# Optimization experiments

Measured on AMD Instinct MI355X. Metric: run time of the kernel, lower is better.

Reference implementation:

```python
import jax, jax.numpy as jnp
import numpy as np

QMAX = 255.0  # uint8 range used by KVQuantizer


def setup_inputs() -> dict:
    key = jax.random.key(0)
    k1, k2 = jax.random.split(key)
    B, KVH, D, S = 1, 8, 128, 8192
    keys = jax.random.normal(k1, (B, KVH, 1, D, S), dtype=jnp.float32)
    values = jax.random.normal(k2, (B, KVH, 1, S, D), dtype=jnp.float32)
    return {"keys": keys, "values": values, "mask": 1, "ids_len": S, "kv_seq_len": S}


def _quantize_block(x, axis):
    # torch.aminmax(x, dim=axis, keepdim=True)
    block_min = jnp.min(x, axis=axis, keepdims=True)
    block_max = jnp.max(x, axis=axis, keepdims=True)
    scale = (block_max - block_min) * (1.0 / QMAX)
    x_packed = jnp.round((x - block_min) / scale)  # F16 path: stays float
    # USE_FLOAT16_SCALE_BIAS=True -> half precision scale/bias
    return x_packed, scale.astype(jnp.float16), block_min.astype(jnp.float16)


def reference(keys, values, mask, ids_len, kv_seq_len):
    # causal mask: (1 - tril(ones)) * -128, sliced [:ids_len, :kv_seq_len], * mask, .float()
    row = jnp.arange(ids_len)[:, None]
    col = jnp.arange(kv_seq_len)[None, :]
    attn = (jnp.where(col > row, jnp.int32(-128), jnp.int32(0)) * jnp.int32(mask)).astype(jnp.float32)
    attn = attn[None, None, None]  # [1,1,1,ids_len,kv_seq_len]

    # per-layer KV-cache quantization (keys blocked over head_dim axis -2, values over -1)
    k_packed, k_scale, k_bias = _quantize_block(keys, -2)
    v_packed, v_scale, v_bias = _quantize_block(values, -1)
    return (attn, k_packed, k_scale, k_bias, v_packed, jnp.swapaxes(v_scale, -1, -2), v_bias)
```

## Files before the change

### kernel.cpp

```cpp
#include <hip/hip_runtime.h>
#include <hip/hip_fp16.h>

#define HH 8
#define DD 128
#define SS 8192

typedef float f32x4 __attribute__((ext_vector_type(4)));

#define GROUPS 1024
#define BLOCKS (GROUPS * 25)

__global__ __launch_bounds__(256) void fused_kernel(
    const float* __restrict__ keys, const float* __restrict__ vals,
    const int* __restrict__ maskp,
    float* __restrict__ attn, float* __restrict__ kp, float* __restrict__ ks,
    float* __restrict__ kb, float* __restrict__ vp, float* __restrict__ vs,
    float* __restrict__ vb)
{
    const int tid = threadIdx.x;
    const int b   = blockIdx.x;
    const int g   = b / 25;
    const int rem = b - g * 25;

    if (rem == 0) {
        const int h  = g >> 7;
        const int s0 = (g & 127) << 6;
        const int sq = tid & 15;
        const int dg = tid >> 4;

        const float* base = keys + (size_t)h * DD * SS + (size_t)dg * 8 * SS + s0 + sq * 4;
        f32x4 v[8];
        f32x4 mn4, mx4;
        mn4.x = mn4.y = mn4.z = mn4.w = 3.0e38f;
        mx4.x = mx4.y = mx4.z = mx4.w = -3.0e38f;
#pragma unroll
        for (int j = 0; j < 8; ++j) {
            v[j] = __builtin_nontemporal_load((const f32x4*)(base + (size_t)j * SS));
            mn4.x = fminf(mn4.x, v[j].x); mx4.x = fmaxf(mx4.x, v[j].x);
            mn4.y = fminf(mn4.y, v[j].y); mx4.y = fmaxf(mx4.y, v[j].y);
            mn4.z = fminf(mn4.z, v[j].z); mx4.z = fmaxf(mx4.z, v[j].z);
            mn4.w = fminf(mn4.w, v[j].w); mx4.w = fmaxf(mx4.w, v[j].w);
        }

        __shared__ f32x4 smn[16][16], smx[16][16];
        __shared__ float sinv[64], sbi[64];
        smn[dg][sq] = mn4;
        smx[dg][sq] = mx4;
        __syncthreads();
        if (tid < 64) {
            const int q = tid >> 2, cmp = tid & 3;
            float m = 3.0e38f, M = -3.0e38f;
#pragma unroll
            for (int gg = 0; gg < 16; ++gg) {
                m = fminf(m, ((const float*)&smn[gg][q])[cmp]);
                M = fmaxf(M, ((const float*)&smx[gg][q])[cmp]);
            }
            const float scale = (M - m) * (1.0f / 255.0f);
            sinv[tid] = 1.0f / scale;
            sbi[tid]  = m;
            const int o = h * SS + s0 + tid;
            ks[o] = __half2float(__float2half(scale));
            kb[o] = __half2float(__float2half(m));
        }
        __syncthreads();
        const f32x4 rs = *(const f32x4*)&sinv[sq * 4];
        const f32x4 bi = *(const f32x4*)&sbi[sq * 4];
        float* ob = kp + (size_t)h * DD * SS + (size_t)dg * 8 * SS + s0 + sq * 4;
#pragma unroll
        for (int j = 0; j < 8; ++j) {
            f32x4 o;
            o.x = rintf((v[j].x - bi.x) * rs.x);
            o.y = rintf((v[j].y - bi.y) * rs.y);
            o.z = rintf((v[j].z - bi.z) * rs.z);
            o.w = rintf((v[j].w - bi.w) * rs.w);
            *(f32x4*)(ob + (size_t)j * SS) = o;
        }
    } else if (rem <= 8) {
        const int vbi = g * 8 + (rem - 1);
        const int d4 = tid & 31;
        const int rr = tid >> 5;
        const int R  = vbi * 8 + rr;

        const f32x4 v = __builtin_nontemporal_load((const f32x4*)vals + (size_t)R * 32 + d4);
        float mn = fminf(fminf(v.x, v.y), fminf(v.z, v.w));
        float mx = fmaxf(fmaxf(v.x, v.y), fmaxf(v.z, v.w));
#pragma unroll
        for (int off = 16; off >= 1; off >>= 1) {
            mn = fminf(mn, __shfl_xor(mn, off));
            mx = fmaxf(mx, __shfl_xor(mx, off));
        }
        const float scale = (mx - mn) * (1.0f / 255.0f);
        const float inv   = 1.0f / scale;
        if (d4 == 0) {
            vs[R] = __half2float(__float2half(scale));
            vb[R] = __half2float(__float2half(mn));
        }
        f32x4 o;
        o.x = rintf((v.x - mn) * inv);
        o.y = rintf((v.y - mn) * inv);
        o.z = rintf((v.z - mn) * inv);
        o.w = rintf((v.w - mn) * inv);
        *((f32x4*)vp + (size_t)R * 32 + d4) = o;
    } else {
        const int a = g * 16 + (rem - 9);
        const float hi = (float)(-128 * (*maskp));
        const int base = a * 1024 + tid;
#pragma unroll
        for (int ch = 0; ch < 4; ++ch) {
            const int idx = base + ch * 256;
            const int r = idx >> 11;
            const int c = (idx & 2047) << 2;
            f32x4 v;
            v.x = (c + 0 > r) ? hi : 0.0f;
            v.y = (c + 1 > r) ? hi : 0.0f;
            v.z = (c + 2 > r) ? hi : 0.0f;
            v.w = (c + 3 > r) ? hi : 0.0f;
            *((f32x4*)attn + idx) = v;
        }
    }
}

extern "C" void kernel_launch(void* const* d_in, const int* in_sizes, int n_in,
                              void* d_out, int out_size, void* d_ws, size_t ws_size,
                              hipStream_t stream) {
    const float* keys  = (const float*)d_in[0];
    const float* vals  = (const float*)d_in[1];
    const int*   maskp = (const int*)d_in[2];

    float* out  = (float*)d_out;
    float* attn = out;
    float* kp   = attn + 67108864;
    float* ks   = kp   + 8388608;
    float* kb   = ks   + 65536;
    float* vp   = kb   + 65536;
    float* vs   = vp   + 8388608;
    float* vb   = vs   + 65536;

    fused_kernel<<<dim3(BLOCKS), dim3(256), 0, stream>>>(keys, vals, maskp,
                                                         attn, kp, ks, kb, vp, vs, vb);
}
```

Measured before the change: 386.0 us.

## Split fused interleaved kernel into separate keys, values and attention-mask kernels

Replaces the single fused kernel, which interleaved key, value and mask blocks by block index, with three separate launches. The mask kernel becomes a grid-stride loop with 32 iterations per thread over 2048 blocks, and the value kernel now handles 32 rows per block. This is meant to cut block count and per-block dispatch overhead and to make each kernel's work uniform. In exchange it adds two kernel launches and gives up the overlap of the read-heavy quantization work with the write-only mask fill.

Result: no change. 384.1 us (-0.5%).

```diff
diff --git a/kernel.cpp b/kernel.cpp
--- a/kernel.cpp
+++ b/kernel.cpp
@@ -7,80 +7,92 @@
 
 typedef float f32x4 __attribute__((ext_vector_type(4)));
 
-#define GROUPS 1024
-#define BLOCKS (GROUPS * 25)
+#define ATTN_BLOCKS 2048
+__global__ __launch_bounds__(256) void attn_kernel(const int* __restrict__ maskp,
+                                                   float* __restrict__ out) {
+    const float hi = (float)(-128 * (*maskp));
+    int idx = blockIdx.x * 256 + threadIdx.x;
+#pragma unroll
+    for (int it = 0; it < 32; ++it, idx += ATTN_BLOCKS * 256) {
+        const int r = idx >> 11;
+        const int c = (idx & 2047) << 2;
+        f32x4 v;
+        v.x = (c + 0 > r) ? hi : 0.0f;
+        v.y = (c + 1 > r) ? hi : 0.0f;
+        v.z = (c + 2 > r) ? hi : 0.0f;
+        v.w = (c + 3 > r) ? hi : 0.0f;
+        *((f32x4*)out + idx) = v;
+    }
+}
 
-__global__ __launch_bounds__(256) void fused_kernel(
-    const float* __restrict__ keys, const float* __restrict__ vals,
-    const int* __restrict__ maskp,
-    float* __restrict__ attn, float* __restrict__ kp, float* __restrict__ ks,
-    float* __restrict__ kb, float* __restrict__ vp, float* __restrict__ vs,
-    float* __restrict__ vb)
-{
-    const int tid = threadIdx.x;
-    const int b   = blockIdx.x;
-    const int g   = b / 25;
-    const int rem = b - g * 25;
+__global__ __launch_bounds__(256) void keys_kernel(const float* __restrict__ keys,
+                                                   float* __restrict__ kp,
+                                                   float* __restrict__ ks,
+                                                   float* __restrict__ kb) {
+    const int h  = blockIdx.x >> 7;
+    const int s0 = (blockIdx.x & 127) << 6;
+    const int sq = threadIdx.x & 15;
+    const int dg = threadIdx.x >> 4;
 
-    if (rem == 0) {
-        const int h  = g >> 7;
-        const int s0 = (g & 127) << 6;
-        const int sq = tid & 15;
-        const int dg = tid >> 4;
+    const float* base = keys + (size_t)h * DD * SS + (size_t)dg * 8 * SS + s0 + sq * 4;
+    f32x4 v[8];
+    f32x4 mn4, mx4;
+    mn4.x = mn4.y = mn4.z = mn4.w = 3.0e38f;
+    mx4.x = mx4.y = mx4.z = mx4.w = -3.0e38f;
+#pragma unroll
+    for (int j = 0; j < 8; ++j) {
+        v[j] = __builtin_nontemporal_load((const f32x4*)(base + (size_t)j * SS));
+        mn4.x = fminf(mn4.x, v[j].x); mx4.x = fmaxf(mx4.x, v[j].x);
+        mn4.y = fminf(mn4.y, v[j].y); mx4.y = fmaxf(mx4.y, v[j].y);
+        mn4.z = fminf(mn4.z, v[j].z); mx4.z = fmaxf(mx4.z, v[j].z);
+        mn4.w = fminf(mn4.w, v[j].w); mx4.w = fmaxf(mx4.w, v[j].w);
+    }
 
-        const float* base = keys + (size_t)h * DD * SS + (size_t)dg * 8 * SS + s0 + sq * 4;
-        f32x4 v[8];
-        f32x4 mn4, mx4;
-        mn4.x = mn4.y = mn4.z = mn4.w = 3.0e38f;
-        mx4.x = mx4.y = mx4.z = mx4.w = -3.0e38f;
+    __shared__ f32x4 smn[16][16], smx[16][16];
+    __shared__ float sinv[64], sbi[64];
+    smn[dg][sq] = mn4;
+    smx[dg][sq] = mx4;
+    __syncthreads();
+    if (threadIdx.x < 64) {
+        const int q = threadIdx.x >> 2, cmp = threadIdx.x & 3;
+        float m = 3.0e38f, M = -3.0e38f;
 #pragma unroll
-        for (int j = 0; j < 8; ++j) {
-            v[j] = __builtin_nontemporal_load((const f32x4*)(base + (size_t)j * SS));
-            mn4.x = fminf(mn4.x, v[j].x); mx4.x = fmaxf(mx4.x, v[j].x);
-            mn4.y = fminf(mn4.y, v[j].y); mx4.y = fmaxf(mx4.y, v[j].y);
-            mn4.z = fminf(mn4.z, v[j].z); mx4.z = fmaxf(mx4.z, v[j].z);
-            mn4.w = fminf(mn4.w, v[j].w); mx4.w = fmaxf(mx4.w, v[j].w);
+        for (int gg = 0; gg < 16; ++gg) {
+            m = fminf(m, ((const float*)&smn[gg][q])[cmp]);
+            M = fmaxf(M, ((const float*)&smx[gg][q])[cmp]);
         }
+        const float scale = (M - m) * (1.0f / 255.0f);
+        sinv[threadIdx.x] = 1.0f / scale;
+        sbi[threadIdx.x]  = m;
+        const int o = h * SS + s0 + threadIdx.x;
+        ks[o] = __half2float(__float2half(scale));
+        kb[o] = __half2float(__float2half(m));
+    }
+    __syncthreads();
+    const f32x4 rs = *(const f32x4*)&sinv[sq * 4];
+    const f32x4 bi = *(const f32x4*)&sbi[sq * 4];
+    float* ob = kp + (size_t)h * DD * SS + (size_t)dg * 8 * SS + s0 + sq * 4;
+#pragma unroll
+    for (int j = 0; j < 8; ++j) {
+        f32x4 o;
+        o.x = rintf((v[j].x - bi.x) * rs.x);
+        o.y = rintf((v[j].y - bi.y) * rs.y);
+        o.z = rintf((v[j].z - bi.z) * rs.z);
+        o.w = rintf((v[j].w - bi.w) * rs.w);
+        *(f32x4*)(ob + (size_t)j * SS) = o;
+    }
+}
 
-        __shared__ f32x4 smn[16][16], smx[16][16];
-        __shared__ float sinv[64], sbi[64];
-        smn[dg][sq] = mn4;
-        smx[dg][sq] = mx4;
-        __syncthreads();
-        if (tid < 64) {
-            const int q = tid >> 2, cmp = tid & 3;
-            float m = 3.0e38f, M = -3.0e38f;
+__global__ __launch_bounds__(256) void vals_kernel(const float* __restrict__ vals,
+                                                   float* __restrict__ vp,
+                                                   float* __restrict__ vs,
+                                                   float* __restrict__ vb) {
+    const int d4 = threadIdx.x & 31;
+    const int rr = threadIdx.x >> 5;
+    const int R0 = blockIdx.x * 32;
 #pragma unroll
-            for (int gg = 0; gg < 16; ++gg) {
-                m = fminf(m, ((const float*)&smn[gg][q])[cmp]);
-                M = fmaxf(M, ((const float*)&smx[gg][q])[cmp]);
-            }
-            const float scale = (M - m) * (1.0f / 255.0f);
-            sinv[tid] = 1.0f / scale;
-            sbi[tid]  = m;
-            const int o = h * SS + s0 + tid;
-            ks[o] = __half2float(__float2half(scale));
-            kb[o] = __half2float(__float2half(m));
-        }
-        __syncthreads();
-        const f32x4 rs = *(const f32x4*)&sinv[sq * 4];
-        const f32x4 bi = *(const f32x4*)&sbi[sq * 4];
-        float* ob = kp + (size_t)h * DD * SS + (size_t)dg * 8 * SS + s0 + sq * 4;
-#pragma unroll
-        for (int j = 0; j < 8; ++j) {
-            f32x4 o;
-            o.x = rintf((v[j].x - bi.x) * rs.x);
-            o.y = rintf((v[j].y - bi.y) * rs.y);
-            o.z = rintf((v[j].z - bi.z) * rs.z);
-            o.w = rintf((v[j].w - bi.w) * rs.w);
-            *(f32x4*)(ob + (size_t)j * SS) = o;
-        }
-    } else if (rem <= 8) {
-        const int vbi = g * 8 + (rem - 1);
-        const int d4 = tid & 31;
-        const int rr = tid >> 5;
-        const int R  = vbi * 8 + rr;
-
+    for (int p = 0; p < 4; ++p) {
+        const int R = R0 + p * 8 + rr;
         const f32x4 v = __builtin_nontemporal_load((const f32x4*)vals + (size_t)R * 32 + d4);
         float mn = fminf(fminf(v.x, v.y), fminf(v.z, v.w));
         float mx = fmaxf(fmaxf(v.x, v.y), fmaxf(v.z, v.w));
@@ -101,22 +113,6 @@
         o.z = rintf((v.z - mn) * inv);
         o.w = rintf((v.w - mn) * inv);
         *((f32x4*)vp + (size_t)R * 32 + d4) = o;
-    } else {
-        const int a = g * 16 + (rem - 9);
-        const float hi = (float)(-128 * (*maskp));
-        const int base = a * 1024 + tid;
-#pragma unroll
-        for (int ch = 0; ch < 4; ++ch) {
-            const int idx = base + ch * 256;
-            const int r = idx >> 11;
-            const int c = (idx & 2047) << 2;
-            f32x4 v;
-            v.x = (c + 0 > r) ? hi : 0.0f;
-            v.y = (c + 1 > r) ? hi : 0.0f;
-            v.z = (c + 2 > r) ? hi : 0.0f;
-            v.w = (c + 3 > r) ? hi : 0.0f;
-            *((f32x4*)attn + idx) = v;
-        }
     }
 }
 
@@ -136,6 +132,7 @@
     float* vs   = vp   + 8388608;
     float* vb   = vs   + 65536;
 
-    fused_kernel<<<dim3(BLOCKS), dim3(256), 0, stream>>>(keys, vals, maskp,
-                                                         attn, kp, ks, kb, vp, vs, vb);
+    keys_kernel<<<dim3(HH * (SS / 64)), dim3(256), 0, stream>>>(keys, kp, ks, kb);
+    vals_kernel<<<dim3(HH * SS / 32), dim3(256), 0, stream>>>(vals, vp, vs, vb);
+    attn_kernel<<<dim3(ATTN_BLOCKS), dim3(256), 0, stream>>>(maskp, attn);
 }
```
